# Kernel optimization log

Measured on AMD Instinct MI355X. Metric: run time of the kernel, lower is better.

Reference implementation:

```python
import jax, jax.numpy as jnp
import numpy as np

B, S, SQ, N, DIN, H, A, O = 32, 1024, 32, 128, 128, 256, 100, 2000
MEM_COUNT, ANS_COUNT = 3, 2


def _gru_cell(x, h, w_ih, w_hh, b_ih, b_hh):
    # PyTorch GRUCell math
    gi = x @ w_ih.T + b_ih
    gh = h @ w_hh.T + b_hh
    i_r, i_z, i_n = jnp.split(gi, 3, axis=-1)
    h_r, h_z, h_n = jnp.split(gh, 3, axis=-1)
    r = jax.nn.sigmoid(i_r + h_r)
    z = jax.nn.sigmoid(i_z + h_z)
    n = jnp.tanh(i_n + r * h_n)
    return (1.0 - z) * n + z * h


def _gru_seq(x, h0, w_ih, w_hh, b_ih, b_hh):
    def step(h, xt):
        hn = _gru_cell(xt, h, w_ih, w_hh, b_ih, b_hh)
        return hn, hn
    hT, ys = jax.lax.scan(step, h0, jnp.swapaxes(x, 0, 1))
    return jnp.swapaxes(ys, 0, 1), hT


def setup_inputs() -> dict:
    key = jax.random.key(0)
    ks = iter(jax.random.split(key, 40))
    def U(shape, a=0.05):
        return jax.random.uniform(next(ks), shape, minval=-a, maxval=a, dtype=jnp.float32)
    inp = {}
    inp['c'] = jax.random.normal(next(ks), (B, S, DIN), dtype=jnp.float32)
    inp['q'] = jax.random.normal(next(ks), (B, SQ, DIN), dtype=jnp.float32)
    inp['i_state'] = jnp.zeros((1, B, H), jnp.float32)
    inp['q_state'] = jnp.zeros((1, B, H), jnp.float32)
    for p in ['in', 'qe']:
        inp[p + '_w_ih'] = U((3 * H, DIN)); inp[p + '_w_hh'] = U((3 * H, H))
        inp[p + '_b_ih'] = U((3 * H,)); inp[p + '_b_hh'] = U((3 * H,))
    inp['att_weight'] = U((H, H))
    inp['att_w1'] = U((A, 7 * H + 2)); inp['att_b1'] = U((A,))
    inp['att_w2'] = U((1, A)); inp['att_b2'] = U((1,))
    inp['mem_w_ih'] = U((3 * H, H)); inp['mem_w_hh'] = U((3 * H, H))
    inp['mem_b_ih'] = U((3 * H,)); inp['mem_b_hh'] = U((3 * H,))
    inp['out_w'] = U((O, H)); inp['out_b'] = U((O,))
    inp['ans_w_ih'] = U((3 * H, O + H)); inp['ans_w_hh'] = U((3 * H, H))
    inp['ans_b_ih'] = U((3 * H,)); inp['ans_b_hh'] = U((3 * H,))
    inp['c_index'] = jnp.sort(jax.random.randint(next(ks), (B, N), 0, S), axis=1)
    inp['len_c'] = jax.random.randint(next(ks), (B,), 1, N + 1)
    return inp


def reference(c, q, i_state, q_state, in_w_ih, in_w_hh, in_b_ih, in_b_hh,
              qe_w_ih, qe_w_hh, qe_b_ih, qe_b_hh, att_weight,
              att_w1, att_b1, att_w2, att_b2,
              mem_w_ih, mem_w_hh, mem_b_ih, mem_b_hh,
              out_w, out_b, ans_w_ih, ans_w_hh, ans_b_ih, ans_b_hh,
              c_index, len_c):
    # input / question GRU encoders (dropout omitted: eval mode)
    c_out, _ = _gru_seq(c, i_state[0], in_w_ih, in_w_hh, in_b_ih, in_b_hh)
    _, q_hT = _gru_seq(q, q_state[0], qe_w_ih, qe_w_hh, qe_b_ih, qe_b_hh)
    q_h = q_hT[:, None, :]                                   # [B,1,H]
    # gather sentence-end hidden states: [B,N,H]
    c_sel = jnp.take_along_axis(c_out, c_index[:, :, None], axis=1)
    n_sent = c_index.shape[1]
    mask = jnp.arange(n_sent)[None, :] < len_c[:, None]      # [B,N]
    cw = c_sel @ att_weight                                   # [B,N,H] (fixed across hops)
    m = q_h
    att_list = []
    for _ in range(MEM_COUNT):
        dot_q = (cw * q_h).sum(-1)                            # [B,N]
        dot_m = (cw * m).sum(-1)                              # [B,N]
        feats = jnp.concatenate([
            c_sel, jnp.broadcast_to(m, c_sel.shape), jnp.broadcast_to(q_h, c_sel.shape),
            c_sel * q_h, c_sel * m, jnp.abs(c_sel - q_h), jnp.abs(c_sel - m),
            dot_q[..., None], dot_m[..., None]], axis=2)      # [B,N,7H+2]
        h1 = jnp.tanh(feats @ att_w1.T + att_b1)
        scores = (h1 @ att_w2.T + att_b2)[..., 0]             # [B,N]
        p = jax.nn.softmax(jnp.where(mask, scores, -jnp.inf), axis=1)
        p = jnp.where(mask, p, 0.0)                           # zero-pad like pad_sequence
        att_list.append(p[..., None])
        e = (c_sel * p[..., None]).sum(1)                     # [B,H]
        m = _gru_cell(e, m[:, 0, :], mem_w_ih, mem_w_hh, mem_b_ih, mem_b_hh)[:, None, :]
    msq = m[:, 0, :]
    for _ in range(ANS_COUNT):
        y = jax.nn.softmax(msq @ out_w.T + out_b, axis=1)
        msq = _gru_cell(jnp.concatenate([y, q_hT], axis=1), msq,
                        ans_w_ih, ans_w_hh, ans_b_ih, ans_b_hh)
    y = jax.nn.softmax(msq @ out_w.T + out_b, axis=1)
    return y, jnp.stack(att_list)
```

## Files before the change

### kernel.cpp

```cpp
#include <hip/hip_runtime.h>
#include <cstdint>
#include <cstddef>

typedef short bf16x8 __attribute__((ext_vector_type(8)));
typedef float f32x4 __attribute__((ext_vector_type(4)));
typedef int   i32x4 __attribute__((ext_vector_type(4)));

#define DEV static __device__ __forceinline__

DEV unsigned short f2bf(float x){
  union{float f; unsigned int u;} v; v.f = x;
  unsigned int r = (v.u + 0x7FFFu + ((v.u>>16)&1u)) >> 16;
  return (unsigned short)r;
}
DEV float bf2f(unsigned short h){
  union{unsigned int u; float f;} v; v.u = ((unsigned int)h)<<16;
  return v.f;
}
DEV float bfsel(int dw, int hi){
  union{unsigned int u; float f;} v;
  v.u = hi ? ((unsigned int)dw & 0xFFFF0000u) : ((unsigned int)dw << 16);
  return v.f;
}
DEV float sigm_f(float x){ return __builtin_amdgcn_rcpf(1.0f + __expf(-x)); }
DEV float tanh_f(float x){ return 2.0f*__builtin_amdgcn_rcpf(1.0f + __expf(-2.0f*x)) - 1.0f; }

__global__ void k_f2bf(const float* __restrict__ src, unsigned short* __restrict__ dst, int n){
  int i = blockIdx.x*256 + threadIdx.x;
  if(i<n) dst[i] = f2bf(src[i]);
}

__global__ void k_transpose(const float* __restrict__ in, float* __restrict__ out, int R, int C){
  int i = blockIdx.x*256 + threadIdx.x;
  if(i < R*C){ int r = i/C, c = i - r*C; out[(size_t)c*R + r] = in[i]; }
}

__global__ void k_attw1(const float* __restrict__ w1, unsigned short* __restrict__ dst){
  int i = blockIdx.x*256 + threadIdx.x;
  if(i < 128*1824){
    int r = i/1824, cc = i - r*1824;
    float v = (r<100 && cc<1794)? w1[r*1794 + cc] : 0.0f;
    dst[i] = f2bf(v);
  }
}

__global__ void k_attwT(const float* __restrict__ aw, unsigned short* __restrict__ dst){
  int i = blockIdx.x*256 + threadIdx.x;
  if(i<65536){ int n = i>>8, k = i&255; dst[i] = f2bf(aw[k*256 + n]); }
}

__global__ void k_b1pad(const float* __restrict__ b1, float* __restrict__ dst){
  int i = threadIdx.x; if(i<128) dst[i] = (i<100)? b1[i] : 0.0f;
}

__global__ void k_copy(const float* __restrict__ s, float* __restrict__ d, int n){
  int i = blockIdx.x*256+threadIdx.x; if(i<n) d[i]=s[i];
}

__global__ __launch_bounds__(256) void k_gemm_bf16(
    const unsigned short* __restrict__ A, const unsigned short* __restrict__ Bt,
    int K, const float* __restrict__ bias, int act,
    float* __restrict__ outf, unsigned short* __restrict__ outbf, int ldc)
{
  int lane = threadIdx.x & 63, wave = threadIdx.x >> 6;
  int m_base = blockIdx.x*64 + (wave>>1)*32;
  int n_base = blockIdx.y*64 + (wave&1)*32;
  int cl = lane & 15, q4 = lane >> 4;
  f32x4 acc00={0.f,0.f,0.f,0.f}, acc01=acc00, acc10=acc00, acc11=acc00;
  const int kf_n = K >> 5;
  for(int kf=0; kf<kf_n; kf++){
    int ko = kf*32 + q4*8;
    bf16x8 a0 = *(const bf16x8*)(A + (size_t)(m_base+cl)*K + ko);
    bf16x8 a1 = *(const bf16x8*)(A + (size_t)(m_base+16+cl)*K + ko);
    bf16x8 b0 = *(const bf16x8*)(Bt + (size_t)(n_base+cl)*K + ko);
    bf16x8 b1 = *(const bf16x8*)(Bt + (size_t)(n_base+16+cl)*K + ko);
    acc00 = __builtin_amdgcn_mfma_f32_16x16x32_bf16(a0,b0,acc00,0,0,0);
    acc01 = __builtin_amdgcn_mfma_f32_16x16x32_bf16(a0,b1,acc01,0,0,0);
    acc10 = __builtin_amdgcn_mfma_f32_16x16x32_bf16(a1,b0,acc10,0,0,0);
    acc11 = __builtin_amdgcn_mfma_f32_16x16x32_bf16(a1,b1,acc11,0,0,0);
  }
  #pragma unroll
  for(int mt=0; mt<2; mt++){
    #pragma unroll
    for(int nt=0; nt<2; nt++){
      f32x4 av = (mt==0)? (nt==0?acc00:acc01) : (nt==0?acc10:acc11);
      int col = n_base + nt*16 + cl;
      float bv = bias? bias[col] : 0.0f;
      #pragma unroll
      for(int r=0;r<4;r++){
        int row = m_base + mt*16 + q4*4 + r;
        float v = av[r] + bv;
        if(act) v = tanh_f(v);
        if(outbf) outbf[(size_t)row*ldc + col] = f2bf(v);
        else      outf [(size_t)row*ldc + col] = v;
      }
    }
  }
}

__global__ __launch_bounds__(256) void k_gemm_gi(
    const unsigned short* __restrict__ A, const unsigned short* __restrict__ Bt,
    const float* __restrict__ bias, unsigned short* __restrict__ gi_out, int ss)
{
  int lane = threadIdx.x & 63, wave = threadIdx.x >> 6;
  int m_base = blockIdx.x*64 + (wave>>1)*32;
  int n_base = blockIdx.y*64 + (wave&1)*32;
  int cl = lane & 15, q4 = lane >> 4;
  f32x4 acc00={0.f,0.f,0.f,0.f}, acc01=acc00, acc10=acc00, acc11=acc00;
  for(int kf=0; kf<4; kf++){
    int ko = kf*32 + q4*8;
    bf16x8 a0 = *(const bf16x8*)(A + (size_t)(m_base+cl)*128 + ko);
    bf16x8 a1 = *(const bf16x8*)(A + (size_t)(m_base+16+cl)*128 + ko);
    bf16x8 b0 = *(const bf16x8*)(Bt + (size_t)(n_base+cl)*128 + ko);
    bf16x8 b1 = *(const bf16x8*)(Bt + (size_t)(n_base+16+cl)*128 + ko);
    acc00 = __builtin_amdgcn_mfma_f32_16x16x32_bf16(a0,b0,acc00,0,0,0);
    acc01 = __builtin_amdgcn_mfma_f32_16x16x32_bf16(a0,b1,acc01,0,0,0);
    acc10 = __builtin_amdgcn_mfma_f32_16x16x32_bf16(a1,b0,acc10,0,0,0);
    acc11 = __builtin_amdgcn_mfma_f32_16x16x32_bf16(a1,b1,acc11,0,0,0);
  }
  const int tmask = (1<<ss) - 1;
  #pragma unroll
  for(int mt=0; mt<2; mt++){
    #pragma unroll
    for(int nt=0; nt<2; nt++){
      f32x4 av = (mt==0)? (nt==0?acc00:acc01) : (nt==0?acc10:acc11);
      int col = n_base + nt*16 + cl;
      float bv = bias[col];
      int g = col >> 8, rem = col & 255;
      int w = rem >> 5, s = (rem>>4)&1, cl2 = rem & 15;
      #pragma unroll
      for(int r=0;r<4;r++){
        int arow = m_base + mt*16 + q4*4 + r;
        int t = arow & tmask, b = arow >> ss;
        int blk = b >> 4, brow = b & 15;
        int lane2 = (brow>>2)*16 + cl2, rc = brow & 3;
        size_t idx = ((((size_t)t*2 + blk)*8 + w)*64 + lane2)*24 + g*8 + s*4 + rc;
        gi_out[idx] = f2bf(av[r] + bv);
      }
    }
  }
}

__global__ __launch_bounds__(512,1) void k_gru_rec(
    const unsigned short* __restrict__ whh_c, const unsigned short* __restrict__ whh_q,
    const unsigned short* __restrict__ gi_c,  const unsigned short* __restrict__ gi_q,
    const float* __restrict__ bhh_c, const float* __restrict__ bhh_q,
    const float* __restrict__ h0_c,  const float* __restrict__ h0_q,
    float* __restrict__ c_out, float* __restrict__ q_hT)
{
  __shared__ unsigned short hb0[16*264];
  __shared__ unsigned short hb1[16*264];

  const int blk = blockIdx.x;
  const bool isq = blk >= 2;
  const int cls = isq? blk-2 : blk;
  const int b0 = cls * 16;
  const unsigned short* W  = isq? whh_q : whh_c;
  const unsigned short* GI = isq? gi_q  : gi_c;
  const float* bhh = isq? bhh_q : bhh_c;
  const float* h0  = isq? h0_q  : h0_c;
  const int steps  = isq? 32 : 1024;

  const int tid = threadIdx.x;
  const int lane = tid & 63, wave = tid >> 6;
  const int cl = lane & 15, q4 = lane >> 4;

  bf16x8 Bf[3][2][8];
  #pragma unroll
  for(int g=0; g<3; g++)
    #pragma unroll
    for(int s=0; s<2; s++){
      const unsigned short* wrow = W + (size_t)(g*256 + wave*32 + s*16 + cl)*256;
      #pragma unroll
      for(int kf=0; kf<8; kf++)
        Bf[g][s][kf] = *(const bf16x8*)(wrow + kf*32 + q4*8);
    }

  float bR[2], bZ[2], bN[2];
  #pragma unroll
  for(int s=0; s<2; s++){
    const int col = wave*32 + s*16 + cl;
    bR[s] = bhh[col]; bZ[s] = bhh[256+col]; bN[s] = bhh[512+col];
  }

  float hreg[2][4];
  #pragma unroll
  for(int s=0; s<2; s++){
    const int col = wave*32 + s*16 + cl;
    #pragma unroll
    for(int r=0; r<4; r++){
      const int row = q4*4 + r;
      float v = h0[(size_t)(b0+row)*256 + col];
      hreg[s][r] = v;
      hb0[row*264 + col] = f2bf(v);
    }
  }
  __syncthreads();

  unsigned short* hb_rd = hb0;
  unsigned short* hb_wr = hb1;

  const unsigned short* gi_lane = GI + (((size_t)cls*8 + wave)*64 + lane)*24;
  const size_t gi_tstride = (size_t)2*8*64*24;

  for(int t=0; t<steps; t++){
    const unsigned short* gp = gi_lane + (size_t)t*gi_tstride;
    i32x4 G0 = *(const i32x4*)(gp);
    i32x4 G1 = *(const i32x4*)(gp + 8);
    i32x4 G2 = *(const i32x4*)(gp + 16);

    if(!isq && t>0){
      #pragma unroll
      for(int s=0; s<2; s++){
        const int col = wave*32 + s*16 + cl;
        #pragma unroll
        for(int r=0; r<4; r++)
          c_out[((size_t)(b0+q4*4+r)*1024 + (t-1))*256 + col] = hreg[s][r];
      }
    }

    f32x4 acc[3][2];
    #pragma unroll
    for(int g=0; g<3; g++)
      #pragma unroll
      for(int s=0; s<2; s++){ f32x4 z={0.f,0.f,0.f,0.f}; acc[g][s]=z; }
    #pragma unroll
    for(int kf=0; kf<8; kf++){
      bf16x8 a = *(const bf16x8*)&hb_rd[cl*264 + kf*32 + q4*8];
      #pragma unroll
      for(int g=0; g<3; g++)
        #pragma unroll
        for(int s=0; s<2; s++)
          acc[g][s] = __builtin_amdgcn_mfma_f32_16x16x32_bf16(a, Bf[g][s][kf], acc[g][s], 0,0,0);
    }

    #pragma unroll
    for(int s=0; s<2; s++){
      const int col = wave*32 + s*16 + cl;
      #pragma unroll
      for(int r=0; r<4; r++){
        const int row = q4*4 + r;
        const int k = s*4 + r;
        float gir = bfsel(G0[k>>1], k&1);
        float giz = bfsel(G1[k>>1], k&1);
        float gin = bfsel(G2[k>>1], k&1);
        float rr = sigm_f(gir + acc[0][s][r] + bR[s]);
        float zz = sigm_f(giz + acc[1][s][r] + bZ[s]);
        float nn = tanh_f(gin + rr*(acc[2][s][r] + bN[s]));
        float x  = nn + zz*(hreg[s][r] - nn);
        hreg[s][r] = x;
        hb_wr[row*264 + col] = f2bf(x);
      }
    }
    __syncthreads();
    unsigned short* tmp = hb_rd; hb_rd = hb_wr; hb_wr = tmp;
  }

  #pragma unroll
  for(int s=0; s<2; s++){
    const int col = wave*32 + s*16 + cl;
    #pragma unroll
    for(int r=0; r<4; r++){
      const int row = q4*4 + r;
      if(!isq) c_out[((size_t)(b0+row)*1024 + (steps-1))*256 + col] = hreg[s][r];
      else     q_hT[(size_t)(b0+row)*256 + col] = hreg[s][r];
    }
  }
}

__global__ void k_gather(const float* __restrict__ c_out, const int* __restrict__ c_index,
                         float* __restrict__ c_sel, unsigned short* __restrict__ c_sel_bf){
  int row = blockIdx.x;
  int b = row >> 7, s = row & 127;
  int idx = c_index[b*128 + s];
  float v = c_out[((size_t)b*1024 + idx)*256 + threadIdx.x];
  c_sel   [(size_t)row*256 + threadIdx.x] = v;
  c_sel_bf[(size_t)row*256 + threadIdx.x] = f2bf(v);
}

__global__ void k_feats(const float* __restrict__ c_sel, const float* __restrict__ cw,
                        const float* __restrict__ m_, const float* __restrict__ qh,
                        unsigned short* __restrict__ feats){
  int row = blockIdx.x, tid = threadIdx.x;
  int b = row >> 7;
  float cs  = c_sel[(size_t)row*256 + tid];
  float mj  = m_[b*256 + tid];
  float qj  = qh[b*256 + tid];
  float cwj = cw[(size_t)row*256 + tid];
  float dq = cwj*qj, dm = cwj*mj;
  #pragma unroll
  for(int o=32;o>0;o>>=1){ dq += __shfl_down(dq,o); dm += __shfl_down(dm,o); }
  __shared__ float rq[4], rm[4];
  int lane = tid&63, wave=tid>>6;
  if(lane==0){ rq[wave]=dq; rm[wave]=dm; }
  __syncthreads();
  unsigned short* fr = feats + (size_t)row*1824;
  fr[tid]      = f2bf(cs);
  fr[256+tid]  = f2bf(mj);
  fr[512+tid]  = f2bf(qj);
  fr[768+tid]  = f2bf(cs*qj);
  fr[1024+tid] = f2bf(cs*mj);
  fr[1280+tid] = f2bf(fabsf(cs-qj));
  fr[1536+tid] = f2bf(fabsf(cs-mj));
  if(tid==0){
    float DQ = rq[0]+rq[1]+rq[2]+rq[3];
    float DM = rm[0]+rm[1]+rm[2]+rm[3];
    fr[1792]=f2bf(DQ); fr[1793]=f2bf(DM);
  }
  if(tid<30) fr[1794+tid]=0;
}

__global__ void k_scores(const float* __restrict__ h1, const float* __restrict__ w2,
                         const float* __restrict__ b2, float* __restrict__ scores){
  int row = blockIdx.x*4 + (threadIdx.x>>6);
  int lane = threadIdx.x & 63;
  float v = 0.0f;
  if(lane < 100)    v += h1[(size_t)row*128 + lane]*w2[lane];
  if(lane+64 < 100) v += h1[(size_t)row*128 + lane+64]*w2[lane+64];
  #pragma unroll
  for(int o=32;o>0;o>>=1) v += __shfl_down(v,o);
  if(lane==0) scores[row] = v + b2[0];
}

__global__ void k_softmax_e(const float* __restrict__ scores, const int* __restrict__ len_c,
                            const float* __restrict__ c_sel, float* __restrict__ out_att,
                            float* __restrict__ e){
  __shared__ float red[256];
  __shared__ float p[128];
  int b = blockIdx.x, tid = threadIdx.x;
  int L = len_c[b];
  float s = -1e30f;
  if(tid<128 && tid<L) s = scores[b*128+tid];
  red[tid]=s; __syncthreads();
  for(int o=128;o>0;o>>=1){ if(tid<o) red[tid]=fmaxf(red[tid],red[tid+o]); __syncthreads(); }
  float mx = red[0]; __syncthreads();
  float ex = (tid<128 && tid<L)? __expf(s-mx) : 0.0f;
  red[tid]=ex; __syncthreads();
  for(int o=128;o>0;o>>=1){ if(tid<o) red[tid]+=red[tid+o]; __syncthreads(); }
  float inv = 1.0f/red[0];
  if(tid<128){ float pv = ex*inv; p[tid]=pv; out_att[b*128+tid]=pv; }
  __syncthreads();
  float acc = 0.0f;
  for(int si=0; si<128; si++) acc += p[si]*c_sel[((size_t)b*128+si)*256 + tid];
  e[b*256+tid] = acc;
}

__global__ void k_gru_cell(const float* __restrict__ x1, int len1,
                           const float* __restrict__ x2, int len2,
                           const float* __restrict__ hprev,
                           const float* __restrict__ wihT, const float* __restrict__ whhT,
                           const float* __restrict__ bih, const float* __restrict__ bhh,
                           float* __restrict__ hout){
  __shared__ float xs[2304];
  __shared__ float hs[256];
  int m = blockIdx.x, tid = threadIdx.x;
  int Kx = len1 + len2;
  for(int i=tid;i<len1;i+=256) xs[i] = x1[(size_t)m*len1 + i];
  for(int i=tid;i<len2;i+=256) xs[len1+i] = x2[(size_t)m*len2 + i];
  hs[tid] = hprev[m*256 + tid];
  __syncthreads();
  float ar=0, az=0, an=0;
  for(int k=0;k<Kx;k++){
    float xv = xs[k];
    const float* wr = wihT + (size_t)k*768;
    ar += xv*wr[tid]; az += xv*wr[256+tid]; an += xv*wr[512+tid];
  }
  float gr=0, gz=0, gn=0;
  for(int k=0;k<256;k++){
    float hv = hs[k];
    const float* wr = whhT + (size_t)k*768;
    gr += hv*wr[tid]; gz += hv*wr[256+tid]; gn += hv*wr[512+tid];
  }
  float rr = sigm_f(ar + bih[tid]     + gr + bhh[tid]);
  float zz = sigm_f(az + bih[256+tid] + gz + bhh[256+tid]);
  float nn = tanh_f(an + bih[512+tid] + rr*(gn + bhh[512+tid]));
  hout[m*256+tid] = (1.0f-zz)*nn + zz*hs[tid];
}

__global__ void k_logits(const float* __restrict__ msq, const float* __restrict__ out_wT,
                         const float* __restrict__ out_b, float* __restrict__ ylin){
  int i = blockIdx.x*256 + threadIdx.x;
  if(i >= 32*2000) return;
  int mrow = i/2000, n = i - mrow*2000;
  float acc = out_b[n];
  const float* mr = msq + mrow*256;
  for(int k=0;k<256;k++) acc += mr[k]*out_wT[(size_t)k*2000 + n];
  ylin[i] = acc;
}

__global__ void k_softmax_o(const float* __restrict__ x, float* __restrict__ y){
  __shared__ float red[256];
  int b = blockIdx.x, tid = threadIdx.x;
  const float* xr = x + (size_t)b*2000;
  float mx = -1e30f;
  for(int i=tid;i<2000;i+=256) mx = fmaxf(mx, xr[i]);
  red[tid]=mx; __syncthreads();
  for(int o=128;o>0;o>>=1){ if(tid<o) red[tid]=fmaxf(red[tid],red[tid+o]); __syncthreads(); }
  mx = red[0]; __syncthreads();
  float sum=0.0f;
  for(int i=tid;i<2000;i+=256) sum += __expf(xr[i]-mx);
  red[tid]=sum; __syncthreads();
  for(int o=128;o>0;o>>=1){ if(tid<o) red[tid]+=red[tid+o]; __syncthreads(); }
  float inv = 1.0f/red[0];
  for(int i=tid;i<2000;i+=256) y[(size_t)b*2000+i] = __expf(xr[i]-mx)*inv;
}

extern "C" void kernel_launch(void* const* d_in, const int* in_sizes, int n_in,
                              void* d_out, int out_size, void* d_ws, size_t ws_size,
                              hipStream_t stream)
{
  const float* c        = (const float*)d_in[0];
  const float* q        = (const float*)d_in[1];
  const float* i_state  = (const float*)d_in[2];
  const float* q_state  = (const float*)d_in[3];
  const float* in_w_ih  = (const float*)d_in[4];
  const float* in_w_hh  = (const float*)d_in[5];
  const float* in_b_ih  = (const float*)d_in[6];
  const float* in_b_hh  = (const float*)d_in[7];
  const float* qe_w_ih  = (const float*)d_in[8];
  const float* qe_w_hh  = (const float*)d_in[9];
  const float* qe_b_ih  = (const float*)d_in[10];
  const float* qe_b_hh  = (const float*)d_in[11];
  const float* att_weight = (const float*)d_in[12];
  const float* att_w1   = (const float*)d_in[13];
  const float* att_b1   = (const float*)d_in[14];
  const float* att_w2   = (const float*)d_in[15];
  const float* att_b2   = (const float*)d_in[16];
  const float* mem_w_ih = (const float*)d_in[17];
  const float* mem_w_hh = (const float*)d_in[18];
  const float* mem_b_ih = (const float*)d_in[19];
  const float* mem_b_hh = (const float*)d_in[20];
  const float* out_w    = (const float*)d_in[21];
  const float* out_b    = (const float*)d_in[22];
  const float* ans_w_ih = (const float*)d_in[23];
  const float* ans_w_hh = (const float*)d_in[24];
  const float* ans_b_ih = (const float*)d_in[25];
  const float* ans_b_hh = (const float*)d_in[26];
  const int*   c_index  = (const int*)d_in[27];
  const int*   len_c    = (const int*)d_in[28];
  float* outp = (float*)d_out;

  char* wp = (char*)d_ws;
  auto take = [&](size_t nbytes)->char*{
    char* p = wp; wp += (nbytes + 255) & ~(size_t)255; return p;
  };
  unsigned short* c_bf      = (unsigned short*)take((size_t)32*1024*128*2);
  unsigned short* q_bf      = (unsigned short*)take((size_t)32*32*128*2);
  unsigned short* wih_in_bf = (unsigned short*)take(768*128*2);
  unsigned short* wih_qe_bf = (unsigned short*)take(768*128*2);
  unsigned short* whh_in_bf = (unsigned short*)take(768*256*2);
  unsigned short* whh_qe_bf = (unsigned short*)take(768*256*2);
  unsigned short* attwT_bf  = (unsigned short*)take(256*256*2);
  unsigned short* attw1_bf  = (unsigned short*)take(128*1824*2);
  float* b1pad              = (float*)take(128*4);
  float* out_wT             = (float*)take((size_t)256*2000*4);
  float* mem_wihT           = (float*)take(256*768*4);
  float* mem_whhT           = (float*)take(256*768*4);
  float* ans_wihT           = (float*)take((size_t)2256*768*4);
  float* ans_whhT           = (float*)take(256*768*4);
  unsigned short* gi_c_bf   = (unsigned short*)take((size_t)32768*768*2);
  unsigned short* gi_q_bf   = (unsigned short*)take((size_t)1024*768*2);
  float* c_out              = (float*)take((size_t)32*1024*256*4);
  float* q_hT               = (float*)take(32*256*4);
  float* c_sel              = (float*)take((size_t)4096*256*4);
  unsigned short* c_sel_bf  = (unsigned short*)take((size_t)4096*256*2);
  float* cw                 = (float*)take((size_t)4096*256*4);
  unsigned short* feats_bf  = (unsigned short*)take((size_t)4096*1824*2);
  float* h1                 = (float*)take((size_t)4096*128*4);
  float* scores             = (float*)take(4096*4);
  float* e_buf              = (float*)take(32*256*4);
  float* m_buf              = (float*)take(32*256*4);
  float* msq                = (float*)take(32*256*4);
  float* ylin               = (float*)take((size_t)32*2000*4);
  float* ybuf               = (float*)take((size_t)32*2000*4);

  k_f2bf<<<16384,256,0,stream>>>(c, c_bf, 32*1024*128);
  k_f2bf<<<512,256,0,stream>>>(q, q_bf, 32*32*128);
  k_f2bf<<<384,256,0,stream>>>(in_w_ih, wih_in_bf, 768*128);
  k_f2bf<<<384,256,0,stream>>>(qe_w_ih, wih_qe_bf, 768*128);
  k_f2bf<<<768,256,0,stream>>>(in_w_hh, whh_in_bf, 768*256);
  k_f2bf<<<768,256,0,stream>>>(qe_w_hh, whh_qe_bf, 768*256);
  k_attwT<<<256,256,0,stream>>>(att_weight, attwT_bf);
  k_attw1<<<912,256,0,stream>>>(att_w1, attw1_bf);
  k_b1pad<<<1,128,0,stream>>>(att_b1, b1pad);
  k_transpose<<<2000,256,0,stream>>>(out_w, out_wT, 2000, 256);
  k_transpose<<<768,256,0,stream>>>(mem_w_ih, mem_wihT, 768, 256);
  k_transpose<<<768,256,0,stream>>>(mem_w_hh, mem_whhT, 768, 256);
  k_transpose<<<6768,256,0,stream>>>(ans_w_ih, ans_wihT, 768, 2256);
  k_transpose<<<768,256,0,stream>>>(ans_w_hh, ans_whhT, 768, 256);

  k_gemm_gi<<<dim3(512,12),256,0,stream>>>(c_bf, wih_in_bf, in_b_ih, gi_c_bf, 10);
  k_gemm_gi<<<dim3(16,12),256,0,stream>>>(q_bf, wih_qe_bf, qe_b_ih, gi_q_bf, 5);

  k_gru_rec<<<4,512,0,stream>>>(whh_in_bf, whh_qe_bf, gi_c_bf, gi_q_bf,
                                in_b_hh, qe_b_hh, i_state, q_state, c_out, q_hT);

  k_gather<<<4096,256,0,stream>>>(c_out, c_index, c_sel, c_sel_bf);
  k_gemm_bf16<<<dim3(64,4),256,0,stream>>>(c_sel_bf, attwT_bf, 256, nullptr, 0, cw, nullptr, 256);
  k_copy<<<32,256,0,stream>>>(q_hT, m_buf, 32*256);

  for(int it=0; it<3; it++){
    k_feats<<<4096,256,0,stream>>>(c_sel, cw, m_buf, q_hT, feats_bf);
    k_gemm_bf16<<<dim3(64,2),256,0,stream>>>(feats_bf, attw1_bf, 1824, b1pad, 1, h1, nullptr, 128);
    k_scores<<<1024,256,0,stream>>>(h1, att_w2, att_b2, scores);
    k_softmax_e<<<32,256,0,stream>>>(scores, len_c, c_sel, outp + 64000 + it*4096, e_buf);
    k_gru_cell<<<32,256,0,stream>>>(e_buf, 256, nullptr, 0, m_buf,
                                    mem_wihT, mem_whhT, mem_b_ih, mem_b_hh, m_buf);
  }

  k_copy<<<32,256,0,stream>>>(m_buf, msq, 32*256);
  for(int it=0; it<2; it++){
    k_logits<<<250,256,0,stream>>>(msq, out_wT, out_b, ylin);
    k_softmax_o<<<32,256,0,stream>>>(ylin, ybuf);
    k_gru_cell<<<32,256,0,stream>>>(ybuf, 2000, q_hT, 256, msq,
                                    ans_wihT, ans_whhT, ans_b_ih, ans_b_hh, msq);
  }
  k_logits<<<250,256,0,stream>>>(msq, out_wT, out_b, ylin);
  k_softmax_o<<<32,256,0,stream>>>(ylin, outp);
}
```

Baseline: 3.061 ms.

## Fuse attention tail and answer-module kernels into per-batch fused kernels

Merges score dot-product, masked softmax, weighted context sum and the memory GRU cell into one per-batch kernel. It also merges the output logits, softmax and answer GRU cell into a single kernel that keeps the logits in shared memory. The copy kernels go away by pointing the first iteration at q_hT directly. This removes many small launches and global round-trips for intermediates. In exchange the logits GEMV now runs on only 32 blocks instead of 250, which lowers parallelism for that step.

```diff
diff --git a/kernel.cpp b/kernel.cpp
--- a/kernel.cpp
+++ b/kernel.cpp
@@ -51,10 +51,6 @@
 
 __global__ void k_b1pad(const float* __restrict__ b1, float* __restrict__ dst){
   int i = threadIdx.x; if(i<128) dst[i] = (i<100)? b1[i] : 0.0f;
-}
-
-__global__ void k_copy(const float* __restrict__ s, float* __restrict__ d, int n){
-  int i = blockIdx.x*256+threadIdx.x; if(i<n) d[i]=s[i];
 }
 
 __global__ __launch_bounds__(256) void k_gemm_bf16(
@@ -310,27 +306,26 @@
   if(tid<30) fr[1794+tid]=0;
 }
 
-__global__ void k_scores(const float* __restrict__ h1, const float* __restrict__ w2,
-                         const float* __restrict__ b2, float* __restrict__ scores){
-  int row = blockIdx.x*4 + (threadIdx.x>>6);
-  int lane = threadIdx.x & 63;
-  float v = 0.0f;
-  if(lane < 100)    v += h1[(size_t)row*128 + lane]*w2[lane];
-  if(lane+64 < 100) v += h1[(size_t)row*128 + lane+64]*w2[lane+64];
-  #pragma unroll
-  for(int o=32;o>0;o>>=1) v += __shfl_down(v,o);
-  if(lane==0) scores[row] = v + b2[0];
-}
-
-__global__ void k_softmax_e(const float* __restrict__ scores, const int* __restrict__ len_c,
-                            const float* __restrict__ c_sel, float* __restrict__ out_att,
-                            float* __restrict__ e){
+__global__ void k_att_tail(const float* __restrict__ h1, const float* __restrict__ w2,
+                           const float* __restrict__ b2, const int* __restrict__ len_c,
+                           const float* __restrict__ c_sel,
+                           const float* __restrict__ m_in,
+                           const float* __restrict__ wihT, const float* __restrict__ whhT,
+                           const float* __restrict__ bih, const float* __restrict__ bhh,
+                           float* __restrict__ out_att, float* __restrict__ m_out){
   __shared__ float red[256];
   __shared__ float p[128];
+  __shared__ float es[256];
+  __shared__ float hs[256];
   int b = blockIdx.x, tid = threadIdx.x;
   int L = len_c[b];
   float s = -1e30f;
-  if(tid<128 && tid<L) s = scores[b*128+tid];
+  if(tid < 128 && tid < L){
+    const float* hr = h1 + ((size_t)b*128 + tid)*128;
+    float a = 0.0f;
+    for(int k=0;k<100;k++) a += hr[k]*w2[k];
+    s = a + b2[0];
+  }
   red[tid]=s; __syncthreads();
   for(int o=128;o>0;o>>=1){ if(tid<o) red[tid]=fmaxf(red[tid],red[tid+o]); __syncthreads(); }
   float mx = red[0]; __syncthreads();
@@ -339,29 +334,15 @@
   for(int o=128;o>0;o>>=1){ if(tid<o) red[tid]+=red[tid+o]; __syncthreads(); }
   float inv = 1.0f/red[0];
   if(tid<128){ float pv = ex*inv; p[tid]=pv; out_att[b*128+tid]=pv; }
+  hs[tid] = m_in[b*256+tid];
   __syncthreads();
   float acc = 0.0f;
   for(int si=0; si<128; si++) acc += p[si]*c_sel[((size_t)b*128+si)*256 + tid];
-  e[b*256+tid] = acc;
-}
-
-__global__ void k_gru_cell(const float* __restrict__ x1, int len1,
-                           const float* __restrict__ x2, int len2,
-                           const float* __restrict__ hprev,
-                           const float* __restrict__ wihT, const float* __restrict__ whhT,
-                           const float* __restrict__ bih, const float* __restrict__ bhh,
-                           float* __restrict__ hout){
-  __shared__ float xs[2304];
-  __shared__ float hs[256];
-  int m = blockIdx.x, tid = threadIdx.x;
-  int Kx = len1 + len2;
-  for(int i=tid;i<len1;i+=256) xs[i] = x1[(size_t)m*len1 + i];
-  for(int i=tid;i<len2;i+=256) xs[len1+i] = x2[(size_t)m*len2 + i];
-  hs[tid] = hprev[m*256 + tid];
+  es[tid] = acc;
   __syncthreads();
   float ar=0, az=0, an=0;
-  for(int k=0;k<Kx;k++){
-    float xv = xs[k];
+  for(int k=0;k<256;k++){
+    float xv = es[k];
     const float* wr = wihT + (size_t)k*768;
     ar += xv*wr[tid]; az += xv*wr[256+tid]; an += xv*wr[512+tid];
   }
@@ -374,35 +355,66 @@
   float rr = sigm_f(ar + bih[tid]     + gr + bhh[tid]);
   float zz = sigm_f(az + bih[256+tid] + gz + bhh[256+tid]);
   float nn = tanh_f(an + bih[512+tid] + rr*(gn + bhh[512+tid]));
-  hout[m*256+tid] = (1.0f-zz)*nn + zz*hs[tid];
-}
-
-__global__ void k_logits(const float* __restrict__ msq, const float* __restrict__ out_wT,
-                         const float* __restrict__ out_b, float* __restrict__ ylin){
-  int i = blockIdx.x*256 + threadIdx.x;
-  if(i >= 32*2000) return;
-  int mrow = i/2000, n = i - mrow*2000;
-  float acc = out_b[n];
-  const float* mr = msq + mrow*256;
-  for(int k=0;k<256;k++) acc += mr[k]*out_wT[(size_t)k*2000 + n];
-  ylin[i] = acc;
-}
-
-__global__ void k_softmax_o(const float* __restrict__ x, float* __restrict__ y){
+  m_out[b*256+tid] = (1.0f-zz)*nn + zz*hs[tid];
+}
+
+__global__ void k_ans(const float* __restrict__ msq_in, const float* __restrict__ out_wT,
+                      const float* __restrict__ out_b, const float* __restrict__ qh,
+                      const float* __restrict__ wihT, const float* __restrict__ whhT,
+                      const float* __restrict__ bih, const float* __restrict__ bhh,
+                      int do_cell, float* __restrict__ y_out, float* __restrict__ msq_out){
+  __shared__ float yl[2000];
+  __shared__ float ms[256];
+  __shared__ float qs[256];
   __shared__ float red[256];
   int b = blockIdx.x, tid = threadIdx.x;
-  const float* xr = x + (size_t)b*2000;
+  ms[tid] = msq_in[b*256+tid];
+  qs[tid] = qh[b*256+tid];
+  __syncthreads();
+  for(int n=tid; n<2000; n+=256){
+    float acc = out_b[n];
+    for(int k=0;k<256;k++) acc += ms[k]*out_wT[(size_t)k*2000 + n];
+    yl[n] = acc;
+  }
+  __syncthreads();
   float mx = -1e30f;
-  for(int i=tid;i<2000;i+=256) mx = fmaxf(mx, xr[i]);
+  for(int i=tid;i<2000;i+=256) mx = fmaxf(mx, yl[i]);
   red[tid]=mx; __syncthreads();
   for(int o=128;o>0;o>>=1){ if(tid<o) red[tid]=fmaxf(red[tid],red[tid+o]); __syncthreads(); }
   mx = red[0]; __syncthreads();
   float sum=0.0f;
-  for(int i=tid;i<2000;i+=256) sum += __expf(xr[i]-mx);
+  for(int i=tid;i<2000;i+=256) sum += __expf(yl[i]-mx);
   red[tid]=sum; __syncthreads();
   for(int o=128;o>0;o>>=1){ if(tid<o) red[tid]+=red[tid+o]; __syncthreads(); }
   float inv = 1.0f/red[0];
-  for(int i=tid;i<2000;i+=256) y[(size_t)b*2000+i] = __expf(xr[i]-mx)*inv;
+  for(int i=tid;i<2000;i+=256){
+    float yv = __expf(yl[i]-mx)*inv;
+    yl[i] = yv;
+    if(y_out) y_out[(size_t)b*2000+i] = yv;
+  }
+  if(!do_cell) return;
+  __syncthreads();
+  float ar=0, az=0, an=0;
+  for(int k=0;k<2000;k++){
+    float xv = yl[k];
+    const float* wr = wihT + (size_t)k*768;
+    ar += xv*wr[tid]; az += xv*wr[256+tid]; an += xv*wr[512+tid];
+  }
+  for(int k=0;k<256;k++){
+    float xv = qs[k];
+    const float* wr = wihT + (size_t)(2000+k)*768;
+    ar += xv*wr[tid]; az += xv*wr[256+tid]; an += xv*wr[512+tid];
+  }
+  float gr=0, gz=0, gn=0;
+  for(int k=0;k<256;k++){
+    float hv = ms[k];
+    const float* wr = whhT + (size_t)k*768;
+    gr += hv*wr[tid]; gz += hv*wr[256+tid]; gn += hv*wr[512+tid];
+  }
+  float rr = sigm_f(ar + bih[tid]     + gr + bhh[tid]);
+  float zz = sigm_f(az + bih[256+tid] + gz + bhh[256+tid]);
+  float nn = tanh_f(an + bih[512+tid] + rr*(gn + bhh[512+tid]));
+  msq_out[b*256+tid] = (1.0f-zz)*nn + zz*ms[tid];
 }
 
 extern "C" void kernel_launch(void* const* d_in, const int* in_sizes, int n_in,
@@ -467,12 +479,8 @@
   float* cw                 = (float*)take((size_t)4096*256*4);
   unsigned short* feats_bf  = (unsigned short*)take((size_t)4096*1824*2);
   float* h1                 = (float*)take((size_t)4096*128*4);
-  float* scores             = (float*)take(4096*4);
-  float* e_buf              = (float*)take(32*256*4);
   float* m_buf              = (float*)take(32*256*4);
   float* msq                = (float*)take(32*256*4);
-  float* ylin               = (float*)take((size_t)32*2000*4);
-  float* ybuf               = (float*)take((size_t)32*2000*4);
 
   k_f2bf<<<16384,256,0,stream>>>(c, c_bf, 32*1024*128);
   k_f2bf<<<512,256,0,stream>>>(q, q_bf, 32*32*128);
@@ -497,24 +505,23 @@
 
   k_gather<<<4096,256,0,stream>>>(c_out, c_index, c_sel, c_sel_bf);
   k_gemm_bf16<<<dim3(64,4),256,0,stream>>>(c_sel_bf, attwT_bf, 256, nullptr, 0, cw, nullptr, 256);
-  k_copy<<<32,256,0,stream>>>(q_hT, m_buf, 32*256);
 
   for(int it=0; it<3; it++){
-    k_feats<<<4096,256,0,stream>>>(c_sel, cw, m_buf, q_hT, feats_bf);
+    const float* m_cur = (it==0)? q_hT : m_buf;
+    k_feats<<<4096,256,0,stream>>>(c_sel, cw, m_cur, q_hT, feats_bf);
     k_gemm_bf16<<<dim3(64,2),256,0,stream>>>(feats_bf, attw1_bf, 1824, b1pad, 1, h1, nullptr, 128);
-    k_scores<<<1024,256,0,stream>>>(h1, att_w2, att_b2, scores);
-    k_softmax_e<<<32,256,0,stream>>>(scores, len_c, c_sel, outp + 64000 + it*4096, e_buf);
-    k_gru_cell<<<32,256,0,stream>>>(e_buf, 256, nullptr, 0, m_buf,
-                                    mem_wihT, mem_whhT, mem_b_ih, mem_b_hh, m_buf);
-  }
-
-  k_copy<<<32,256,0,stream>>>(m_buf, msq, 32*256);
-  for(int it=0; it<2; it++){
-    k_logits<<<250,256,0,stream>>>(msq, out_wT, out_b, ylin);
-    k_softmax_o<<<32,256,0,stream>>>(ylin, ybuf);
-    k_gru_cell<<<32,256,0,stream>>>(ybuf, 2000, q_hT, 256, msq,
-                                    ans_wihT, ans_whhT, ans_b_ih, ans_b_hh, msq);
-  }
-  k_logits<<<250,256,0,stream>>>(msq, out_wT, out_b, ylin);
-  k_softmax_o<<<32,256,0,stream>>>(ylin, outp);
-}
+    k_att_tail<<<32,256,0,stream>>>(h1, att_w2, att_b2, len_c, c_sel, m_cur,
+                                    mem_wihT, mem_whhT, mem_b_ih, mem_b_hh,
+                                    outp + 64000 + it*4096, m_buf);
+  }
+
+  k_ans<<<32,256,0,stream>>>(m_buf, out_wT, out_b, q_hT,
+                             ans_wihT, ans_whhT, ans_b_ih, ans_b_hh,
+                             1, nullptr, msq);
+  k_ans<<<32,256,0,stream>>>(msq, out_wT, out_b, q_hT,
+                             ans_wihT, ans_whhT, ans_b_ih, ans_b_hh,
+                             1, nullptr, msq);
+  k_ans<<<32,256,0,stream>>>(msq, out_wT, out_b, q_hT,
+                             ans_wihT, ans_whhT, ans_b_ih, ans_b_hh,
+                             0, outp, nullptr);
+}
```

Result: faster. 2.957 ms (-3.4%).
